# Kernel tuning notes

Measured on AMD Instinct MI355X. Metric: run time of the kernel, lower is better.

Reference implementation:

```python
import jax, jax.numpy as jnp
import numpy as np

# --- SARRenderParams (defaults) ---
INC_DEG = 30.0      # incidence angle theta
AZ_DEG = 0.0        # squint azimuth phi
ALT = 5000.0        # radar altitude H
NR = 512            # range samples (image H)
NA = 512            # azimuth samples (image W)
RHO_R = 1.0         # range resolution m/px
RHO_A = 1.0         # azimuth resolution m/px
EPS = 1e-6

BETA = float(np.arcsin(np.clip(np.sin(np.deg2rad(INC_DEG)) * np.cos(np.deg2rad(AZ_DEG)), -1.0, 1.0)))
RC = ALT / np.cos(BETA)                      # reference slant range
_cb, _sb = np.cos(BETA), np.sin(BETA)
# R_w2r with alpha=0 (track angle)
R_W2R = np.array([[1.0, 0.0, 0.0],
                  [0.0, -_cb, -_sb],
                  [0.0, _sb, -_cb]], dtype=np.float32)
RADAR_POS = np.array([0.0, -ALT * np.tan(BETA), ALT], dtype=np.float32)

N_GAUSS = 1024
CHUNK = 128  # Gaussians rendered per scan step (bounds peak memory)


def setup_inputs() -> dict:
    key = jax.random.key(0)
    k1, k2, k3 = jax.random.split(key, 3)
    positions = jax.random.normal(k1, (N_GAUSS, 3), dtype=jnp.float32) * 100.0
    L = jax.random.normal(k2, (N_GAUSS, 3, 3), dtype=jnp.float32)
    cov_world = jnp.einsum('nij,nkj->nik', L, L) + 0.5 * jnp.eye(3, dtype=jnp.float32)  # PD
    intensities = jax.random.uniform(k3, (N_GAUSS,), dtype=jnp.float32)
    return {"positions": positions, "cov_world": cov_world, "intensities": intensities}


def reference(positions, cov_world, intensities):
    R = jnp.asarray(R_W2R)
    p_radar = jnp.asarray(RADAR_POS)
    # world -> radar coordinates: P_r = R (P_w - P_radar)
    pr = (positions - p_radar) @ R.T                         # [N,3]
    cov_r = jnp.einsum('ij,njk,lk->nil', R, cov_world, R)    # [N,3,3]

    Xr, Yr, Zr = pr[:, 0], pr[:, 1], pr[:, 2]
    Rmin = jnp.sqrt(Yr**2 + Zr**2 + EPS**2)                  # [N]
    rc = Rmin / RHO_R + NR / 2.0 - RC / RHO_R                # row center
    cc = Xr / RHO_A + NA / 2.0                               # col center

    # IPP Jacobian J = [[0, Yr/(rho_r Rmin), Zr/(rho_r Rmin)], [1/rho_a, 0, 0]]
    N = positions.shape[0]
    J = jnp.zeros((N, 2, 3), positions.dtype)
    J = (J.at[:, 0, 1].set(Yr / (RHO_R * Rmin))
          .at[:, 0, 2].set(Zr / (RHO_R * Rmin))
          .at[:, 1, 0].set(1.0 / RHO_A))
    cov2 = jnp.einsum('nij,njk,nlk->nil', J, cov_r, J) + 1e-4 * jnp.eye(2, dtype=positions.dtype)

    # analytic 2x2 inverse / det
    a, b, d = cov2[:, 0, 0], cov2[:, 0, 1], cov2[:, 1, 1]
    det = a * d - b * b
    ia, ib, id_ = d / det, -b / det, a / det
    weight = intensities / (2.0 * jnp.pi * det)              # normalized amplitude

    rows = jnp.arange(NR, dtype=positions.dtype)
    cols = jnp.arange(NA, dtype=positions.dtype)

    def body(img, chunk):
        r_c, c_c, ia_c, ib_c, id_c, w_c = chunk              # each [CHUNK]
        dr = rows[None, :] - r_c[:, None]                    # [C,H]
        dc = cols[None, :] - c_c[:, None]                    # [C,W]
        mahal = (ia_c[:, None, None] * dr[:, :, None] ** 2
                 + 2.0 * ib_c[:, None, None] * dr[:, :, None] * dc[:, None, :]
                 + id_c[:, None, None] * dc[:, None, :] ** 2)  # [C,H,W]
        img = img + jnp.einsum('n,nhw->hw', w_c, jnp.exp(-0.5 * mahal))
        return img, None

    chunks = tuple(x.reshape(-1, CHUNK) for x in (rc, cc, ia, ib, id_, weight))
    img, _ = jax.lax.scan(body, jnp.zeros((NR, NA), positions.dtype), chunks)
    return img
```

## Files before the change

kernel.cpp:

```cpp
#include <hip/hip_runtime.h>
#include <math.h>

#define NRR 512
#define NAA 512
#define NG  1024
#define TILE 16
#define TDIM 32
#define NT (TDIM*TDIM)
#define MCUT 40.0f

__device__ constexpr float CB = 0.86602540378443864676f;
__device__ constexpr float SB = 0.5f;
__device__ constexpr float RADAR_Y = -2886.7513459481288f;
__device__ constexpr float RADAR_Z = 5000.0f;
__device__ constexpr float RC_F = 5773.5026918962574f;
__device__ constexpr float KLOG = 0.72134752044448170367f;
__device__ constexpr float INV2PI = 0.15915494309189535f;

#if __has_builtin(__builtin_amdgcn_exp2f)
#define EXP2F(x) __builtin_amdgcn_exp2f(x)
#else
#define EXP2F(x) __expf((x) * 0.6931471805599453094f)
#endif

__device__ __forceinline__ void precompute_one(
    const float* __restrict__ pos, const float* __restrict__ cov,
    const float* __restrict__ inten, int n,
    float& rc, float& cc, float& A, float& B2, float& D, float& w,
    float& a_out, float& d_out) {
    float qx = pos[n * 3 + 0];
    float qy = pos[n * 3 + 1] - RADAR_Y;
    float qz = pos[n * 3 + 2] - RADAR_Z;
    float Xr = qx;
    float Yr = -CB * qy - SB * qz;
    float Zr =  SB * qy - CB * qz;

    const float* C = cov + n * 9;
    float C00 = C[0], C01 = C[1], C02 = C[2];
    float C11 = C[4], C12 = C[5], C22 = C[8];
    float c00p = C00;
    float c01p = -CB * C01 - SB * C02;
    float c02p =  SB * C01 - CB * C02;
    float c11p = CB * CB * C11 + 2.0f * CB * SB * C12 + SB * SB * C22;
    float c12p = CB * SB * (C22 - C11) + (CB * CB - SB * SB) * C12;
    float c22p = SB * SB * C11 - 2.0f * SB * CB * C12 + CB * CB * C22;

    float R2   = Yr * Yr + Zr * Zr + 1e-12f;
    float Rmin = sqrtf(R2);
    rc = (Rmin + 256.0f) - RC_F;
    cc = Xr + 256.0f;

    float a = (Yr * Yr * c11p + 2.0f * Yr * Zr * c12p + Zr * Zr * c22p) / R2 + 1e-4f;
    float b = (Yr * c01p + Zr * c02p) / Rmin;
    float d = c00p + 1e-4f;

    float det = a * d - b * b;
    float inv = 1.0f / det;
    A  = -KLOG * d * inv;
    B2 =  2.0f * KLOG * b * inv;
    D  = -KLOG * a * inv;
    w  = inten[n] * INV2PI * inv;
    a_out = a; d_out = d;
}

__global__ __launch_bounds__(256) void sar_fused(const float* __restrict__ pos,
                                                 const float* __restrict__ cov,
                                                 const float* __restrict__ inten,
                                                 float* __restrict__ out) {
    __shared__ float4 s_p[2 * NG];
    __shared__ int    s_cnt;

    const int tx = blockIdx.x & (TDIM - 1);
    const int ty = blockIdx.x >> 5;
    const float c0 = (float)(tx * TILE);
    const float r0 = (float)(ty * TILE);

    if (threadIdx.x == 0) s_cnt = 0;
    __syncthreads();

#pragma unroll
    for (int k = 0; k < NG / 256; ++k) {
        int n = threadIdx.x + k * 256;
        float rc, cc, A, B2, D, w, a, d;
        precompute_one(pos, cov, inten, n, rc, cc, A, B2, D, w, a, d);
        float dR = sqrtf(MCUT * a);
        float dC = sqrtf(MCUT * d);
        bool hit = (w >= 1e-11f) &
                   (rc + dR >= r0) & (rc - dR <= r0 + (TILE - 1)) &
                   (cc + dC >= c0) & (cc - dC <= c0 + (TILE - 1));
        if (hit) {
            int i = atomicAdd(&s_cnt, 1);
            s_p[2 * i]     = make_float4(rc, cc, A, B2);
            s_p[2 * i + 1] = make_float4(D, w, 0.0f, 0.0f);
        }
    }
    __syncthreads();

    const int m  = s_cnt;
    const int lc = threadIdx.x & (TILE - 1);
    const int lr = threadIdx.x >> 4;
    const float cf = c0 + (float)lc;
    const float rf = r0 + (float)lr;

    float acc = 0.0f;
#pragma unroll 2
    for (int i = 0; i < m; ++i) {
        float4 p0 = s_p[2 * i];
        float4 p1 = s_p[2 * i + 1];
        float dr = rf - p0.x;
        float dc = cf - p0.y;
        float e = fmaf(dr, fmaf(p0.z, dr, p0.w * dc), p1.x * dc * dc);
        acc = fmaf(p1.y, EXP2F(e), acc);
    }
    out[(size_t)(ty * TILE + lr) * NAA + (tx * TILE + lc)] = acc;
}

extern "C" void kernel_launch(void* const* d_in, const int* in_sizes, int n_in,
                              void* d_out, int out_size, void* d_ws, size_t ws_size,
                              hipStream_t stream) {
    const float* pos   = (const float*)d_in[0];
    const float* cov   = (const float*)d_in[1];
    const float* inten = (const float*)d_in[2];
    float* out = (float*)d_out;
    (void)d_ws; (void)ws_size;

    sar_fused<<<dim3(NT), dim3(256), 0, stream>>>(pos, cov, inten, out);
}
```

Baseline: 61.97 us.

## Split per-Gaussian precompute into separate kernel, cull from workspace in splat

Adds a small precompute kernel that projects each Gaussian once and writes culling bounds and conic parameters to workspace. The splat kernel then reads these float4s instead of recomputing the projection of all 1024 Gaussians in each of the 1024 tiles. This removes work that was repeated across every block, at the cost of an extra launch and a global-memory round trip. The fused kernel is kept as a fallback when the workspace is too small.

```diff
diff --git a/kernel.cpp b/kernel.cpp
--- a/kernel.cpp
+++ b/kernel.cpp
@@ -63,9 +63,24 @@
     a_out = a; d_out = d;
 }
 
-__global__ __launch_bounds__(256) void sar_fused(const float* __restrict__ pos,
-                                                 const float* __restrict__ cov,
-                                                 const float* __restrict__ inten,
+__global__ void sar_precompute(const float* __restrict__ pos,
+                               const float* __restrict__ cov,
+                               const float* __restrict__ inten,
+                               float4* __restrict__ cull,
+                               float4* __restrict__ par) {
+    int n = blockIdx.x * blockDim.x + threadIdx.x;
+    if (n >= NG) return;
+    float rc, cc, A, B2, D, w, a, d;
+    precompute_one(pos, cov, inten, n, rc, cc, A, B2, D, w, a, d);
+    float dR = sqrtf(MCUT * a);
+    float dC = sqrtf(MCUT * d);
+    if (w < 1e-11f) { dR = -1.0f; dC = -1.0f; }
+    cull[n] = make_float4(rc, cc, dR, dC);
+    par[n]  = make_float4(A, B2, D, w);
+}
+
+__global__ __launch_bounds__(256) void sar_splat(const float4* __restrict__ cull,
+                                                 const float4* __restrict__ par,
                                                  float* __restrict__ out) {
     __shared__ float4 s_p[2 * NG];
     __shared__ int    s_cnt;
@@ -81,17 +96,14 @@
 #pragma unroll
     for (int k = 0; k < NG / 256; ++k) {
         int n = threadIdx.x + k * 256;
-        float rc, cc, A, B2, D, w, a, d;
-        precompute_one(pos, cov, inten, n, rc, cc, A, B2, D, w, a, d);
-        float dR = sqrtf(MCUT * a);
-        float dC = sqrtf(MCUT * d);
-        bool hit = (w >= 1e-11f) &
-                   (rc + dR >= r0) & (rc - dR <= r0 + (TILE - 1)) &
-                   (cc + dC >= c0) & (cc - dC <= c0 + (TILE - 1));
+        float4 q = cull[n];
+        bool hit = (q.x + q.z >= r0) & (q.x - q.z <= r0 + (TILE - 1)) &
+                   (q.y + q.w >= c0) & (q.y - q.w <= c0 + (TILE - 1));
         if (hit) {
+            float4 p = par[n];
             int i = atomicAdd(&s_cnt, 1);
-            s_p[2 * i]     = make_float4(rc, cc, A, B2);
-            s_p[2 * i + 1] = make_float4(D, w, 0.0f, 0.0f);
+            s_p[2 * i]     = make_float4(q.x, q.y, p.x, p.y);
+            s_p[2 * i + 1] = make_float4(p.z, p.w, 0.0f, 0.0f);
         }
     }
     __syncthreads();
@@ -115,6 +127,53 @@
     out[(size_t)(ty * TILE + lr) * NAA + (tx * TILE + lc)] = acc;
 }
 
+__global__ __launch_bounds__(256) void sar_fused(const float* __restrict__ pos,
+                                                 const float* __restrict__ cov,
+                                                 const float* __restrict__ inten,
+                                                 float* __restrict__ out) {
+    __shared__ float4 s_p[2 * NG];
+    __shared__ int    s_cnt;
+    const int tx = blockIdx.x & (TDIM - 1);
+    const int ty = blockIdx.x >> 5;
+    const float c0 = (float)(tx * TILE);
+    const float r0 = (float)(ty * TILE);
+    if (threadIdx.x == 0) s_cnt = 0;
+    __syncthreads();
+#pragma unroll
+    for (int k = 0; k < NG / 256; ++k) {
+        int n = threadIdx.x + k * 256;
+        float rc, cc, A, B2, D, w, a, d;
+        precompute_one(pos, cov, inten, n, rc, cc, A, B2, D, w, a, d);
+        float dR = sqrtf(MCUT * a);
+        float dC = sqrtf(MCUT * d);
+        bool hit = (w >= 1e-11f) &
+                   (rc + dR >= r0) & (rc - dR <= r0 + (TILE - 1)) &
+                   (cc + dC >= c0) & (cc - dC <= c0 + (TILE - 1));
+        if (hit) {
+            int i = atomicAdd(&s_cnt, 1);
+            s_p[2 * i]     = make_float4(rc, cc, A, B2);
+            s_p[2 * i + 1] = make_float4(D, w, 0.0f, 0.0f);
+        }
+    }
+    __syncthreads();
+    const int m  = s_cnt;
+    const int lc = threadIdx.x & (TILE - 1);
+    const int lr = threadIdx.x >> 4;
+    const float cf = c0 + (float)lc;
+    const float rf = r0 + (float)lr;
+    float acc = 0.0f;
+#pragma unroll 2
+    for (int i = 0; i < m; ++i) {
+        float4 p0 = s_p[2 * i];
+        float4 p1 = s_p[2 * i + 1];
+        float dr = rf - p0.x;
+        float dc = cf - p0.y;
+        float e = fmaf(dr, fmaf(p0.z, dr, p0.w * dc), p1.x * dc * dc);
+        acc = fmaf(p1.y, EXP2F(e), acc);
+    }
+    out[(size_t)(ty * TILE + lr) * NAA + (tx * TILE + lc)] = acc;
+}
+
 extern "C" void kernel_launch(void* const* d_in, const int* in_sizes, int n_in,
                               void* d_out, int out_size, void* d_ws, size_t ws_size,
                               hipStream_t stream) {
@@ -122,7 +181,14 @@
     const float* cov   = (const float*)d_in[1];
     const float* inten = (const float*)d_in[2];
     float* out = (float*)d_out;
-    (void)d_ws; (void)ws_size;
 
-    sar_fused<<<dim3(NT), dim3(256), 0, stream>>>(pos, cov, inten, out);
+    if (ws_size >= 2 * NG * sizeof(float4)) {
+        float4* cull = (float4*)d_ws;
+        float4* par  = cull + NG;
+        sar_precompute<<<dim3((NG + 255) / 256), dim3(256), 0, stream>>>(
+            pos, cov, inten, cull, par);
+        sar_splat<<<dim3(NT), dim3(256), 0, stream>>>(cull, par, out);
+    } else {
+        sar_fused<<<dim3(NT), dim3(256), 0, stream>>>(pos, cov, inten, out);
+    }
 }
```

Result: no change. 61.96 us (-0.0%).
